# Kernel tuning notes

Hardware: AMD Instinct MI355X
Metric: run time of the kernel (lower is better)

## Reference

```python
import jax, jax.numpy as jnp
import numpy as np

N = 100000        # nodes
E = 1600000       # directed edges (before self loops)
F = 128           # input node features
H1, H2, H3 = 64, 32, 16
G = 64            # graphs in batch
EPS = 1e-5
NEG_SLOPE = 0.2


def setup_inputs():
    key = jax.random.key(0)
    ks = jax.random.split(key, 16)
    def rn(k, shape, scale=1.0):
        return jax.random.normal(k, shape, dtype=jnp.float32) * scale
    inp = {}
    inp['x'] = rn(ks[0], (N, F))
    inp['edge_index'] = jax.random.randint(ks[1], (2, E), 0, N)
    inp['batch'] = jnp.sort(jax.random.randint(ks[2], (N,), 0, G))
    dims = [(F, H1), (H1, H2), (H2, H3)]
    i = 3
    for li, (fi, fo) in enumerate(dims, start=1):
        s = 1.0 / np.sqrt(fi)
        kk = jax.random.split(ks[i], 3)
        inp[f'Wl{li}'] = rn(kk[0], (fi, fo), s)
        inp[f'bl{li}'] = jnp.zeros((fo,), jnp.float32)
        inp[f'Wr{li}'] = rn(kk[1], (fi, fo), s)
        inp[f'br{li}'] = jnp.zeros((fo,), jnp.float32)
        inp[f'att{li}'] = rn(kk[2], (fo,), 1.0 / np.sqrt(fo))
        inp[f'bias{li}'] = jnp.zeros((fo,), jnp.float32)
        inp[f'gamma{li}'] = jnp.ones((fo,), jnp.float32)
        inp[f'beta{li}'] = jnp.zeros((fo,), jnp.float32)
        i += 1
    inp['linW'] = rn(ks[i], (H3, 1), 0.25)
    inp['linb'] = jnp.zeros((1,), jnp.float32)
    return inp


def _gatv2(x, Wl, bl, Wr, br, att, bias, src, dst):
    # PyG GATv2Conv, heads=1: e_ij = a^T LeakyReLU(Wl x_j + Wr x_i)
    xl = x @ Wl + bl                         # [N, H] source transform
    xr = x @ Wr + br                         # [N, H] target transform
    e = jax.nn.leaky_relu(xl[src] + xr[dst], NEG_SLOPE) @ att   # [E']
    # numerically stable segment softmax over incoming edges of dst
    emax = jax.ops.segment_max(e, dst, num_segments=N)
    w = jnp.exp(e - emax[dst])
    denom = jax.ops.segment_sum(w, dst, num_segments=N)
    alpha = w / (denom[dst] + 1e-16)         # [E']
    out = jax.ops.segment_sum(alpha[:, None] * xl[src], dst, num_segments=N)
    return out + bias


def _batchnorm(x, gamma, beta):
    mu = jnp.mean(x, axis=0)
    var = jnp.var(x, axis=0)
    return (x - mu) * jax.lax.rsqrt(var + EPS) * gamma + beta


def reference(x, edge_index, batch,
              Wl1, bl1, Wr1, br1, att1, bias1, gamma1, beta1,
              Wl2, bl2, Wr2, br2, att2, bias2, gamma2, beta2,
              Wl3, bl3, Wr3, br3, att3, bias3, gamma3, beta3,
              linW, linb):
    # add self loops once (PyG GATv2Conv default add_self_loops=True)
    loops = jnp.arange(N, dtype=edge_index.dtype)
    src = jnp.concatenate([edge_index[0], loops])
    dst = jnp.concatenate([edge_index[1], loops])

    h = _gatv2(x, Wl1, bl1, Wr1, br1, att1, bias1, src, dst)
    h = jax.nn.relu(_batchnorm(h, gamma1, beta1))
    h = _gatv2(h, Wl2, bl2, Wr2, br2, att2, bias2, src, dst)
    h = jax.nn.relu(_batchnorm(h, gamma2, beta2))
    h = _gatv2(h, Wl3, bl3, Wr3, br3, att3, bias3, src, dst)
    h = jax.nn.relu(_batchnorm(h, gamma3, beta3))

    # global mean pool over graphs
    sums = jax.ops.segment_sum(h, batch, num_segments=G)          # [G, 16]
    cnts = jax.ops.segment_sum(jnp.ones((N,), h.dtype), batch, num_segments=G)
    pooled = sums / jnp.maximum(cnts, 1.0)[:, None]
    return pooled @ linW + linb                                   # [G, 1]
```

## Files before the change

kernel.cpp:

```cpp
#include <hip/hip_runtime.h>
#include <hip/hip_bf16.h>


static constexpr int G_ = 64;

typedef short bfrag __attribute__((ext_vector_type(8)));
typedef float facc  __attribute__((ext_vector_type(4)));

__device__ __forceinline__ float asfloat_(unsigned int u) {
  union { unsigned int i; float f; } c; c.i = u; return c.f;
}
__device__ __forceinline__ unsigned short f2bf(float f) {
  union { float f; unsigned int i; } c;
  c.f = f;
  unsigned int r = c.i + 0x7FFFu + ((c.i >> 16) & 1u);
  return (unsigned short)(r >> 16);
}

__device__ __forceinline__ void load_bf4(const unsigned short* p, float* f) {
  uint2 q = *reinterpret_cast<const uint2*>(p);
  f[0] = asfloat_(q.x << 16); f[1] = asfloat_(q.x & 0xFFFF0000u);
  f[2] = asfloat_(q.y << 16); f[3] = asfloat_(q.y & 0xFFFF0000u);
}

__global__ __launch_bounds__(256) void pack_all(
    const float* __restrict__ Wl1, const float* __restrict__ Wr1,
    const float* __restrict__ bl1, const float* __restrict__ br1,
    const float* __restrict__ Wl2, const float* __restrict__ Wr2,
    const float* __restrict__ bl2, const float* __restrict__ br2,
    const float* __restrict__ Wl3, const float* __restrict__ Wr3,
    const float* __restrict__ bl3, const float* __restrict__ br3,
    unsigned short* __restrict__ Wt1, float* __restrict__ bc1,
    unsigned short* __restrict__ Wt2, float* __restrict__ bc2,
    unsigned short* __restrict__ Wt3, float* __restrict__ bc3) {
  int i = blockIdx.x * 256 + threadIdx.x;
  if (i < 128 * 128) { int c = i >> 7, k = i & 127;
    Wt1[i] = f2bf((c < 64) ? Wl1[k * 64 + c] : Wr1[k * 64 + (c - 64)]); }
  if (i < 128) bc1[i] = (i < 64) ? bl1[i] : br1[i - 64];
  if (i < 64 * 64) { int c = i >> 6, k = i & 63;
    Wt2[i] = f2bf((c < 32) ? Wl2[k * 32 + c] : Wr2[k * 32 + (c - 32)]); }
  if (i < 64) bc2[i] = (i < 32) ? bl2[i] : br2[i - 32];
  if (i < 32 * 32) { int c = i >> 5, k = i & 31;
    Wt3[i] = f2bf((c < 16) ? Wl3[k * 16 + c] : Wr3[k * 16 + (c - 16)]); }
  if (i < 32) bc3[i] = (i < 16) ? bl3[i] : br3[i - 16];
}

__global__ __launch_bounds__(256) void edge_hist(
    const int* __restrict__ ei, int* __restrict__ deg, int E, int Etot, int N) {
  int p = blockIdx.x & 7;
  int q = blockIdx.x >> 3;
  int nbq = gridDim.x >> 3;
  float scale = 8.0f / (float)N;
  for (int i = q * 256 + threadIdx.x; i < Etot; i += nbq * 256) {
    int dst = (i < E) ? ei[E + i] : (i - E);
    int pp = min((int)((float)dst * scale), 7);
    if (pp == p) atomicAdd(&deg[dst], 1);
  }
}

__global__ __launch_bounds__(256) void scan1(
    const int* __restrict__ deg, int* __restrict__ part, int* __restrict__ bsums, int n) {
  __shared__ int ts[256];
  int t = threadIdx.x, b = blockIdx.x;
  int base = b * 1024 + t * 4;
  int d[4];
#pragma unroll
  for (int q = 0; q < 4; q++) d[q] = (base + q < n) ? deg[base + q] : 0;
  int s = d[0] + d[1] + d[2] + d[3];
  ts[t] = s;
  __syncthreads();
  for (int o = 1; o < 256; o <<= 1) {
    int v = (t >= o) ? ts[t - o] : 0;
    __syncthreads();
    ts[t] += v;
    __syncthreads();
  }
  int incl = ts[t];
  if (t == 255) bsums[b] = incl;
  int run = incl - s;
#pragma unroll
  for (int q = 0; q < 4; q++) {
    if (base + q < n) part[base + q] = run;
    run += d[q];
  }
}

__global__ void scan2(int* bsums, int nb) {
  __shared__ int s[256];
  int t = threadIdx.x;
  int v = (t < nb) ? bsums[t] : 0;
  s[t] = v;
  __syncthreads();
  for (int o = 1; o < 256; o <<= 1) {
    int u = (t >= o) ? s[t - o] : 0;
    __syncthreads();
    s[t] += u;
    __syncthreads();
  }
  if (t < nb) bsums[t] = s[t] - v;
}

__global__ __launch_bounds__(256) void scan3(
    int* __restrict__ rp, int* __restrict__ cur, const int* __restrict__ bsums,
    int n, int Etot) {
  int i = blockIdx.x * 256 + threadIdx.x;
  if (i < n) {
    int v = rp[i] + bsums[i >> 10];
    rp[i] = v; cur[i] = v;
  }
  if (i == 0) rp[n] = Etot;
}

__global__ __launch_bounds__(256) void scatter_edges(
    const int* __restrict__ ei, int* __restrict__ cur, int* __restrict__ ssrc,
    int E, int Etot, int N) {
  int p = blockIdx.x & 7;
  int q = blockIdx.x >> 3;
  int nbq = gridDim.x >> 3;
  float scale = 8.0f / (float)N;
  for (int i = q * 256 + threadIdx.x; i < Etot; i += nbq * 256) {
    int dst = (i < E) ? ei[E + i] : (i - E);
    int pp = min((int)((float)dst * scale), 7);
    if (pp != p) continue;
    int src = (i < E) ? ei[i] : (i - E);
    int pos = atomicAdd(&cur[dst], 1);
    ssrc[pos] = src;
  }
}

template <int FI, int FO, int AMODE>
__global__ __launch_bounds__(256) void gemm_mfma(
    const void* __restrict__ Ain, const float* __restrict__ ssb,
    const unsigned short* __restrict__ Wt, const float* __restrict__ bcat,
    unsigned short* __restrict__ XL, unsigned short* __restrict__ XR, int N) {
  constexpr int NT = FO / 16;
  constexpr int KS = FI / 32;
  constexpr int H = FO / 2;
  int tid = threadIdx.x;
  int w = tid >> 6;
  int lr = tid & 15;
  int lg = (tid & 63) >> 4;
  int n0 = blockIdx.x * 64;
  int arow = min(n0 + w * 16 + lr, N - 1);

  facc acc[NT];
#pragma unroll
  for (int t = 0; t < NT; t++)
#pragma unroll
    for (int e = 0; e < 4; e++) acc[t][e] = 0.f;

#pragma unroll
  for (int ks = 0; ks < KS; ks++) {
    int k0 = ks * 32 + lg * 8;
    bfrag a;
    if constexpr (AMODE == 0) {
      const unsigned short* Ab = (const unsigned short*)Ain;
      a = *reinterpret_cast<const bfrag*>(&Ab[(size_t)arow * FI + k0]);
    } else {
      const float* Af = (const float*)Ain;
      const float* p = &Af[(size_t)arow * FI + k0];
      float4 lo = *reinterpret_cast<const float4*>(p);
      float4 hi = *reinterpret_cast<const float4*>(p + 4);
      float f[8] = {lo.x, lo.y, lo.z, lo.w, hi.x, hi.y, hi.z, hi.w};
      if constexpr (AMODE == 2) {
        float4 sc0 = *reinterpret_cast<const float4*>(&ssb[k0]);
        float4 sc1 = *reinterpret_cast<const float4*>(&ssb[k0 + 4]);
        float4 sh0 = *reinterpret_cast<const float4*>(&ssb[FI + k0]);
        float4 sh1 = *reinterpret_cast<const float4*>(&ssb[FI + k0 + 4]);
        float sc[8] = {sc0.x, sc0.y, sc0.z, sc0.w, sc1.x, sc1.y, sc1.z, sc1.w};
        float sh[8] = {sh0.x, sh0.y, sh0.z, sh0.w, sh1.x, sh1.y, sh1.z, sh1.w};
#pragma unroll
        for (int e = 0; e < 8; e++) f[e] = fmaxf(fmaf(f[e], sc[e], sh[e]), 0.f);
      }
      union { bfrag v; unsigned short u[8]; } cv;
#pragma unroll
      for (int e = 0; e < 8; e++) cv.u[e] = f2bf(f[e]);
      a = cv.v;
    }
#pragma unroll
    for (int t = 0; t < NT; t++) {
      bfrag b = *reinterpret_cast<const bfrag*>(&Wt[(size_t)(t * 16 + lr) * FI + k0]);
      acc[t] = __builtin_amdgcn_mfma_f32_16x16x32_bf16(a, b, acc[t], 0, 0, 0);
    }
  }

#pragma unroll
  for (int t = 0; t < NT; t++) {
    int col = t * 16 + lr;
    float bias = bcat[col];
    unsigned short* dstbuf = (t < NT / 2) ? XL : XR;
    int cc = (t < NT / 2) ? col : (col - H);
#pragma unroll
    for (int r = 0; r < 4; r++) {
      int n = n0 + w * 16 + lg * 4 + r;
      if (n < N) dstbuf[(size_t)n * H + cc] = f2bf(acc[t][r] + bias);
    }
  }
}

__device__ __forceinline__ float lrelu02(float z) {
  return fmaxf(z, 0.2f * z);
}

template <int H, bool UN2>
__global__ __launch_bounds__(256) void gat_agg4(
    const unsigned short* __restrict__ XL, const unsigned short* __restrict__ XR,
    const float* __restrict__ att, const float* __restrict__ bias,
    const int* __restrict__ rp, const int* __restrict__ ssrc,
    float* __restrict__ out, int N) {
  constexpr int L = H / 4;
  constexpr int C = 64 / L;
  constexpr int STEP = UN2 ? 2 * C : C;
  int v = blockIdx.x * 4 + (threadIdx.x >> 6);
  if (v >= N) return;
  int lane = threadIdx.x & 63;
  int fl = lane % L;
  int sub = lane / L;

  float xr[4];
  load_bf4(&XR[(size_t)v * H + fl * 4], xr);
  const float4 a4 = *reinterpret_cast<const float4*>(&att[fl * 4]);
  int beg = rp[v], end = rp[v + 1];

  float mA = -3.0e38f, dA = 0.f, accA[4] = {0.f, 0.f, 0.f, 0.f};
  float mB = -3.0e38f, dB = 0.f, accB[4] = {0.f, 0.f, 0.f, 0.f};

  auto edge = [&](int j, float& m, float& d, float (&acc)[4]) {
    int u = ssrc[j];
    float xl[4];
    load_bf4(&XL[(size_t)u * H + fl * 4], xl);
    float t = a4.x * lrelu02(xl[0] + xr[0]);
    t = fmaf(a4.y, lrelu02(xl[1] + xr[1]), t);
    t = fmaf(a4.z, lrelu02(xl[2] + xr[2]), t);
    t = fmaf(a4.w, lrelu02(xl[3] + xr[3]), t);
#pragma unroll
    for (int o = L / 2; o >= 1; o >>= 1) t += __shfl_xor(t, o);
    float diff = t - m;
    if (diff > 8.f) {
      float sc = __expf(-diff);
      d *= sc;
#pragma unroll
      for (int e = 0; e < 4; e++) acc[e] *= sc;
      m = t; diff = 0.f;
    }
    float w = __expf(diff);
    d += w;
#pragma unroll
    for (int e = 0; e < 4; e++) acc[e] = fmaf(w, xl[e], acc[e]);
  };

  for (int j = beg + sub; j < end; j += STEP) {
    edge(j, mA, dA, accA);
    if (UN2) {
      int j2 = j + C;
      if (j2 < end) edge(j2, mB, dB, accB);
    }
  }

  if (UN2) {
    float mn = fmaxf(mA, mB);
    float s1 = __expf(mA - mn), s2 = __expf(mB - mn);
    dA = dA * s1 + dB * s2;
#pragma unroll
    for (int e = 0; e < 4; e++) accA[e] = accA[e] * s1 + accB[e] * s2;
    mA = mn;
  }

#pragma unroll
  for (int o = L; o < 64; o <<= 1) {
    float mo = __shfl_xor(mA, o);
    float d2 = __shfl_xor(dA, o);
    float a0 = __shfl_xor(accA[0], o);
    float a1 = __shfl_xor(accA[1], o);
    float a2 = __shfl_xor(accA[2], o);
    float a3 = __shfl_xor(accA[3], o);
    float mn = fmaxf(mA, mo);
    float s1 = __expf(mA - mn), s2 = __expf(mo - mn);
    dA = dA * s1 + d2 * s2;
    accA[0] = accA[0] * s1 + a0 * s2;
    accA[1] = accA[1] * s1 + a1 * s2;
    accA[2] = accA[2] * s1 + a2 * s2;
    accA[3] = accA[3] * s1 + a3 * s2;
    mA = mn;
  }

  if (lane < L) {
    float inv = 1.f / (dA + 1e-16f);
    const float4 b4 = *reinterpret_cast<const float4*>(&bias[fl * 4]);
    float4 o4 = make_float4(fmaf(accA[0], inv, b4.x), fmaf(accA[1], inv, b4.y),
                            fmaf(accA[2], inv, b4.z), fmaf(accA[3], inv, b4.w));
    *reinterpret_cast<float4*>(&out[(size_t)v * H + fl * 4]) = o4;
  }
}

template <int H>
__global__ __launch_bounds__(256) void bn_stats(
    const float* __restrict__ X, float* __restrict__ stats, int N) {
  __shared__ float ls[256], ls2[256];
  int tid = threadIdx.x;
  int h = tid % H;
  constexpr int RPB = 256 / H;
  int r0 = blockIdx.x * RPB + tid / H;
  float s = 0.f, s2 = 0.f;
  for (int n = r0; n < N; n += gridDim.x * RPB) {
    float val = X[(size_t)n * H + h];
    s += val; s2 += val * val;
  }
  ls[tid] = s; ls2[tid] = s2;
  __syncthreads();
  if (tid < H) {
    for (int g = 1; g < RPB; g++) { s += ls[tid + g * H]; s2 += ls2[tid + g * H]; }
    atomicAdd(&stats[h], s);
    atomicAdd(&stats[H + h], s2);
  }
}

__global__ void bn_finalize(
    const float* __restrict__ stats, const float* __restrict__ gamma,
    const float* __restrict__ beta, float* __restrict__ ss, int H, int N) {
  int h = threadIdx.x;
  if (h < H) {
    float mean = stats[h] / (float)N;
    float var = stats[H + h] / (float)N - mean * mean;
    float istd = rsqrtf(var + 1e-5f);
    float sc = gamma[h] * istd;
    ss[h] = sc;
    ss[H + h] = beta[h] - mean * sc;
  }
}

__global__ __launch_bounds__(256) void pool_kernel(
    const float* __restrict__ X, const float* __restrict__ ss,
    const int* __restrict__ batch, float* __restrict__ pool,
    float* __restrict__ cnt, int N) {
  __shared__ float lp[G_ * 16];
  __shared__ float lc[G_];
  int tid = threadIdx.x;
  for (int j = tid; j < G_ * 16; j += 256) lp[j] = 0.f;
  if (tid < G_) lc[tid] = 0.f;
  __syncthreads();
  int tot = N * 16;
  for (int i = blockIdx.x * 256 + tid; i < tot; i += gridDim.x * 256) {
    int n = i >> 4, h = i & 15;
    int g = batch[n];
    float t = X[i] * ss[h] + ss[16 + h];
    t = (t > 0.f) ? t : 0.f;
    atomicAdd(&lp[g * 16 + h], t);
    if (h == 0) atomicAdd(&lc[g], 1.0f);
  }
  __syncthreads();
  for (int j = tid; j < G_ * 16; j += 256) atomicAdd(&pool[j], lp[j]);
  if (tid < G_) atomicAdd(&cnt[tid], lc[tid]);
}

__global__ void final_linear(
    const float* __restrict__ pool, const float* __restrict__ cnt,
    const float* __restrict__ linW, const float* __restrict__ linb,
    float* __restrict__ out) {
  int g = threadIdx.x;
  if (g < G_) {
    float c = fmaxf(cnt[g], 1.0f);
    float acc = 0.f;
    for (int h = 0; h < 16; h++) acc += (pool[g * 16 + h] / c) * linW[h];
    out[g] = acc + linb[0];
  }
}

extern "C" void kernel_launch(void* const* d_in, const int* in_sizes, int n_in,
                              void* d_out, int out_size, void* d_ws, size_t ws_size,
                              hipStream_t stream) {
  const float* x = (const float*)d_in[0];
  const int* ei = (const int*)d_in[1];
  const int* batch = (const int*)d_in[2];
  const int N = in_sizes[0] / 128;
  const int E = in_sizes[1] / 2;
  const int Etot = E + N;

  char* wsb = (char*)d_ws;
  size_t off = 0;
  auto alloc = [&](size_t bytes) -> void* {
    void* p = wsb + off;
    off += (bytes + 255) & ~(size_t)255;
    return p;
  };
  unsigned short* XLb = (unsigned short*)alloc((size_t)64 * N * 2);
  unsigned short* XRb = (unsigned short*)alloc((size_t)64 * N * 2);
  float* R2 = (float*)alloc((size_t)64 * N * 4);
  int* row_ptr = (int*)alloc((size_t)(N + 1) * 4);
  int* cursor = (int*)alloc((size_t)N * 4);
  int* bsums = (int*)alloc(4096);
  int* ssrc = (int*)alloc((size_t)Etot * 4);
  unsigned short* Wt1 = (unsigned short*)alloc(16384 * 2);
  float* bc1 = (float*)alloc(128 * 4);
  unsigned short* Wt2 = (unsigned short*)alloc(4096 * 2);
  float* bc2 = (float*)alloc(64 * 4);
  unsigned short* Wt3 = (unsigned short*)alloc(1024 * 2);
  float* bc3 = (float*)alloc(32 * 4);
  float* ss = (float*)alloc(256 * 4);
  size_t zelems = (size_t)N + 3 * 128 + G_ * 16 + G_;
  char* zb = (char*)alloc(zelems * 4);
  int* deg = (int*)zb;
  float* stats1 = (float*)(zb + (size_t)N * 4);
  float* stats2 = stats1 + 128;
  float* stats3 = stats2 + 128;
  float* pool = stats3 + 128;
  float* cnt = pool + G_ * 16;

  const float* Wl1 = (const float*)d_in[3];  const float* bl1 = (const float*)d_in[4];
  const float* Wr1 = (const float*)d_in[5];  const float* br1 = (const float*)d_in[6];
  const float* att1 = (const float*)d_in[7]; const float* bias1 = (const float*)d_in[8];
  const float* g1 = (const float*)d_in[9];   const float* b1 = (const float*)d_in[10];
  const float* Wl2 = (const float*)d_in[11]; const float* bl2 = (const float*)d_in[12];
  const float* Wr2 = (const float*)d_in[13]; const float* br2 = (const float*)d_in[14];
  const float* att2 = (const float*)d_in[15]; const float* bias2 = (const float*)d_in[16];
  const float* g2 = (const float*)d_in[17];  const float* b2 = (const float*)d_in[18];
  const float* Wl3 = (const float*)d_in[19]; const float* bl3 = (const float*)d_in[20];
  const float* Wr3 = (const float*)d_in[21]; const float* br3 = (const float*)d_in[22];
  const float* att3 = (const float*)d_in[23]; const float* bias3 = (const float*)d_in[24];
  const float* g3 = (const float*)d_in[25];  const float* b3 = (const float*)d_in[26];
  const float* linW = (const float*)d_in[27]; const float* linb = (const float*)d_in[28];
  float* out = (float*)d_out;

  int nb = (N + 1023) / 1024;
  int nnodeblk = (N + 3) / 4;
  int ngemm = (N + 63) / 64;

  pack_all<<<64, 256, 0, stream>>>(Wl1, Wr1, bl1, br1, Wl2, Wr2, bl2, br2,
                                   Wl3, Wr3, bl3, br3, Wt1, bc1, Wt2, bc2, Wt3, bc3);
  hipMemsetAsync(zb, 0, zelems * 4, stream);

  edge_hist<<<4096, 256, 0, stream>>>(ei, deg, E, Etot, N);
  scan1<<<nb, 256, 0, stream>>>(deg, row_ptr, bsums, N);
  scan2<<<1, 256, 0, stream>>>(bsums, nb);
  scan3<<<(N + 255) / 256, 256, 0, stream>>>(row_ptr, cursor, bsums, N, Etot);
  scatter_edges<<<4096, 256, 0, stream>>>(ei, cursor, ssrc, E, Etot, N);

  gemm_mfma<128, 128, 1><<<ngemm, 256, 0, stream>>>(x, nullptr, Wt1, bc1, XLb, XRb, N);
  gat_agg4<64, true><<<nnodeblk, 256, 0, stream>>>(XLb, XRb, att1, bias1, row_ptr, ssrc, R2, N);
  bn_stats<64><<<512, 256, 0, stream>>>(R2, stats1, N);
  bn_finalize<<<1, 64, 0, stream>>>(stats1, g1, b1, ss, 64, N);

  gemm_mfma<64, 64, 2><<<ngemm, 256, 0, stream>>>(R2, ss, Wt2, bc2, XLb, XRb, N);
  gat_agg4<32, true><<<nnodeblk, 256, 0, stream>>>(XLb, XRb, att2, bias2, row_ptr, ssrc, R2, N);
  bn_stats<32><<<512, 256, 0, stream>>>(R2, stats2, N);
  bn_finalize<<<1, 64, 0, stream>>>(stats2, g2, b2, ss, 32, N);

  gemm_mfma<32, 32, 2><<<ngemm, 256, 0, stream>>>(R2, ss, Wt3, bc3, XLb, XRb, N);
  gat_agg4<16, false><<<nnodeblk, 256, 0, stream>>>(XLb, XRb, att3, bias3, row_ptr, ssrc, R2, N);
  bn_stats<16><<<512, 256, 0, stream>>>(R2, stats3, N);
  bn_finalize<<<1, 64, 0, stream>>>(stats3, g3, b3, ss, 16, N);

  pool_kernel<<<2048, 256, 0, stream>>>(R2, ss, batch, pool, cnt, N);
  final_linear<<<1, 64, 0, stream>>>(pool, cnt, linW, linb, out);
}
```

Measured before the change: 510.1 us.

## Replace online softmax in GAT aggregation with chunked two-pass LDS softmax

```diff
diff --git a/kernel.cpp b/kernel.cpp
--- a/kernel.cpp
+++ b/kernel.cpp
@@ -202,16 +202,18 @@
   return fmaxf(z, 0.2f * z);
 }
 
-template <int H, bool UN2>
-__global__ __launch_bounds__(256) void gat_agg4(
+template <int H>
+__global__ __launch_bounds__(256) void gat_agg5(
     const unsigned short* __restrict__ XL, const unsigned short* __restrict__ XR,
     const float* __restrict__ att, const float* __restrict__ bias,
     const int* __restrict__ rp, const int* __restrict__ ssrc,
     float* __restrict__ out, int N) {
   constexpr int L = H / 4;
   constexpr int C = 64 / L;
-  constexpr int STEP = UN2 ? 2 * C : C;
-  int v = blockIdx.x * 4 + (threadIdx.x >> 6);
+  constexpr int CHUNK = 128;
+  __shared__ float ts[4][CHUNK];
+  int wv = threadIdx.x >> 6;
+  int v = blockIdx.x * 4 + wv;
   if (v >= N) return;
   int lane = threadIdx.x & 63;
   int fl = lane % L;
@@ -222,73 +224,66 @@
   const float4 a4 = *reinterpret_cast<const float4*>(&att[fl * 4]);
   int beg = rp[v], end = rp[v + 1];
 
-  float mA = -3.0e38f, dA = 0.f, accA[4] = {0.f, 0.f, 0.f, 0.f};
-  float mB = -3.0e38f, dB = 0.f, accB[4] = {0.f, 0.f, 0.f, 0.f};
-
-  auto edge = [&](int j, float& m, float& d, float (&acc)[4]) {
-    int u = ssrc[j];
-    float xl[4];
-    load_bf4(&XL[(size_t)u * H + fl * 4], xl);
-    float t = a4.x * lrelu02(xl[0] + xr[0]);
-    t = fmaf(a4.y, lrelu02(xl[1] + xr[1]), t);
-    t = fmaf(a4.z, lrelu02(xl[2] + xr[2]), t);
-    t = fmaf(a4.w, lrelu02(xl[3] + xr[3]), t);
-#pragma unroll
-    for (int o = L / 2; o >= 1; o >>= 1) t += __shfl_xor(t, o);
-    float diff = t - m;
-    if (diff > 8.f) {
-      float sc = __expf(-diff);
-      d *= sc;
-#pragma unroll
-      for (int e = 0; e < 4; e++) acc[e] *= sc;
-      m = t; diff = 0.f;
-    }
-    float w = __expf(diff);
-    d += w;
-#pragma unroll
-    for (int e = 0; e < 4; e++) acc[e] = fmaf(w, xl[e], acc[e]);
-  };
-
-  for (int j = beg + sub; j < end; j += STEP) {
-    edge(j, mA, dA, accA);
-    if (UN2) {
-      int j2 = j + C;
-      if (j2 < end) edge(j2, mB, dB, accB);
-    }
-  }
-
-  if (UN2) {
-    float mn = fmaxf(mA, mB);
-    float s1 = __expf(mA - mn), s2 = __expf(mB - mn);
-    dA = dA * s1 + dB * s2;
-#pragma unroll
-    for (int e = 0; e < 4; e++) accA[e] = accA[e] * s1 + accB[e] * s2;
-    mA = mn;
+  float m = -3.0e38f, d = 0.f, acc[4] = {0.f, 0.f, 0.f, 0.f};
+
+  for (int c0 = beg; c0 < end; c0 += CHUNK) {
+    int n = min(CHUNK, end - c0);
+
+    float mc = -3.0e38f;
+    for (int k = sub; k < n; k += C) {
+      int u = ssrc[c0 + k];
+      float xl[4];
+      load_bf4(&XL[(size_t)u * H + fl * 4], xl);
+      float t = a4.x * lrelu02(xl[0] + xr[0]);
+      t = fmaf(a4.y, lrelu02(xl[1] + xr[1]), t);
+      t = fmaf(a4.z, lrelu02(xl[2] + xr[2]), t);
+      t = fmaf(a4.w, lrelu02(xl[3] + xr[3]), t);
+#pragma unroll
+      for (int o = L / 2; o >= 1; o >>= 1) t += __shfl_xor(t, o);
+      mc = fmaxf(mc, t);
+      if (fl == 0) ts[wv][k] = t;
+    }
+#pragma unroll
+    for (int o = L; o < 64; o <<= 1) mc = fmaxf(mc, __shfl_xor(mc, o));
+
+    float mn = fmaxf(m, mc);
+    float sc = __expf(m - mn);
+    d *= sc;
+#pragma unroll
+    for (int e = 0; e < 4; e++) acc[e] *= sc;
+    m = mn;
+
+    float dl = 0.f;
+    for (int k = lane; k < n; k += 64) {
+      float w = __expf(ts[wv][k] - m);
+      ts[wv][k] = w;
+      dl += w;
+    }
+#pragma unroll
+    for (int o = 1; o < 64; o <<= 1) dl += __shfl_xor(dl, o);
+    d += dl;
+
+    for (int k = sub; k < n; k += C) {
+      float wgt = ts[wv][k];
+      int u = ssrc[c0 + k];
+      float xl[4];
+      load_bf4(&XL[(size_t)u * H + fl * 4], xl);
+#pragma unroll
+      for (int e = 0; e < 4; e++) acc[e] = fmaf(wgt, xl[e], acc[e]);
+    }
   }
 
 #pragma unroll
   for (int o = L; o < 64; o <<= 1) {
-    float mo = __shfl_xor(mA, o);
-    float d2 = __shfl_xor(dA, o);
-    float a0 = __shfl_xor(accA[0], o);
-    float a1 = __shfl_xor(accA[1], o);
-    float a2 = __shfl_xor(accA[2], o);
-    float a3 = __shfl_xor(accA[3], o);
-    float mn = fmaxf(mA, mo);
-    float s1 = __expf(mA - mn), s2 = __expf(mo - mn);
-    dA = dA * s1 + d2 * s2;
-    accA[0] = accA[0] * s1 + a0 * s2;
-    accA[1] = accA[1] * s1 + a1 * s2;
-    accA[2] = accA[2] * s1 + a2 * s2;
-    accA[3] = accA[3] * s1 + a3 * s2;
-    mA = mn;
+#pragma unroll
+    for (int e = 0; e < 4; e++) acc[e] += __shfl_xor(acc[e], o);
   }
 
   if (lane < L) {
-    float inv = 1.f / (dA + 1e-16f);
+    float inv = 1.f / (d + 1e-16f);
     const float4 b4 = *reinterpret_cast<const float4*>(&bias[fl * 4]);
-    float4 o4 = make_float4(fmaf(accA[0], inv, b4.x), fmaf(accA[1], inv, b4.y),
-                            fmaf(accA[2], inv, b4.z), fmaf(accA[3], inv, b4.w));
+    float4 o4 = make_float4(fmaf(acc[0], inv, b4.x), fmaf(acc[1], inv, b4.y),
+                            fmaf(acc[2], inv, b4.z), fmaf(acc[3], inv, b4.w));
     *reinterpret_cast<float4*>(&out[(size_t)v * H + fl * 4]) = o4;
   }
 }
@@ -436,17 +431,17 @@
   scatter_edges<<<4096, 256, 0, stream>>>(ei, cursor, ssrc, E, Etot, N);
 
   gemm_mfma<128, 128, 1><<<ngemm, 256, 0, stream>>>(x, nullptr, Wt1, bc1, XLb, XRb, N);
-  gat_agg4<64, true><<<nnodeblk, 256, 0, stream>>>(XLb, XRb, att1, bias1, row_ptr, ssrc, R2, N);
+  gat_agg5<64><<<nnodeblk, 256, 0, stream>>>(XLb, XRb, att1, bias1, row_ptr, ssrc, R2, N);
   bn_stats<64><<<512, 256, 0, stream>>>(R2, stats1, N);
   bn_finalize<<<1, 64, 0, stream>>>(stats1, g1, b1, ss, 64, N);
 
   gemm_mfma<64, 64, 2><<<ngemm, 256, 0, stream>>>(R2, ss, Wt2, bc2, XLb, XRb, N);
-  gat_agg4<32, true><<<nnodeblk, 256, 0, stream>>>(XLb, XRb, att2, bias2, row_ptr, ssrc, R2, N);
+  gat_agg5<32><<<nnodeblk, 256, 0, stream>>>(XLb, XRb, att2, bias2, row_ptr, ssrc, R2, N);
   bn_stats<32><<<512, 256, 0, stream>>>(R2, stats2, N);
   bn_finalize<<<1, 64, 0, stream>>>(stats2, g2, b2, ss, 32, N);
 
   gemm_mfma<32, 32, 2><<<ngemm, 256, 0, stream>>>(R2, ss, Wt3, bc3, XLb, XRb, N);
-  gat_agg4<16, false><<<nnodeblk, 256, 0, stream>>>(XLb, XRb, att3, bias3, row_ptr, ssrc, R2, N);
+  gat_agg5<16><<<nnodeblk, 256, 0, stream>>>(XLb, XRb, att3, bias3, row_ptr, ssrc, R2, N);
   bn_stats<16><<<512, 256, 0, stream>>>(R2, stats3, N);
   bn_finalize<<<1, 64, 0, stream>>>(stats3, g3, b3, ss, 16, N);
 
```

After: 578.3 us. +13.4%, slower.

## Add chunked batch-load GAT aggregation kernel for layers two and three

Applied to the files above, without the earlier changes.

```diff
diff --git a/kernel.cpp b/kernel.cpp
--- a/kernel.cpp
+++ b/kernel.cpp
@@ -152,31 +152,26 @@
 #pragma unroll
   for (int ks = 0; ks < KS; ks++) {
     int k0 = ks * 32 + lg * 8;
+    const float* Af = (const float*)Ain;
+    const float* p = &Af[(size_t)arow * FI + k0];
+    float4 lo = *reinterpret_cast<const float4*>(p);
+    float4 hi = *reinterpret_cast<const float4*>(p + 4);
+    float f[8] = {lo.x, lo.y, lo.z, lo.w, hi.x, hi.y, hi.z, hi.w};
+    if constexpr (AMODE == 2) {
+      float4 sc0 = *reinterpret_cast<const float4*>(&ssb[k0]);
+      float4 sc1 = *reinterpret_cast<const float4*>(&ssb[k0 + 4]);
+      float4 sh0 = *reinterpret_cast<const float4*>(&ssb[FI + k0]);
+      float4 sh1 = *reinterpret_cast<const float4*>(&ssb[FI + k0 + 4]);
+      float sc[8] = {sc0.x, sc0.y, sc0.z, sc0.w, sc1.x, sc1.y, sc1.z, sc1.w};
+      float sh[8] = {sh0.x, sh0.y, sh0.z, sh0.w, sh1.x, sh1.y, sh1.z, sh1.w};
+#pragma unroll
+      for (int e = 0; e < 8; e++) f[e] = fmaxf(fmaf(f[e], sc[e], sh[e]), 0.f);
+    }
     bfrag a;
-    if constexpr (AMODE == 0) {
-      const unsigned short* Ab = (const unsigned short*)Ain;
-      a = *reinterpret_cast<const bfrag*>(&Ab[(size_t)arow * FI + k0]);
-    } else {
-      const float* Af = (const float*)Ain;
-      const float* p = &Af[(size_t)arow * FI + k0];
-      float4 lo = *reinterpret_cast<const float4*>(p);
-      float4 hi = *reinterpret_cast<const float4*>(p + 4);
-      float f[8] = {lo.x, lo.y, lo.z, lo.w, hi.x, hi.y, hi.z, hi.w};
-      if constexpr (AMODE == 2) {
-        float4 sc0 = *reinterpret_cast<const float4*>(&ssb[k0]);
-        float4 sc1 = *reinterpret_cast<const float4*>(&ssb[k0 + 4]);
-        float4 sh0 = *reinterpret_cast<const float4*>(&ssb[FI + k0]);
-        float4 sh1 = *reinterpret_cast<const float4*>(&ssb[FI + k0 + 4]);
-        float sc[8] = {sc0.x, sc0.y, sc0.z, sc0.w, sc1.x, sc1.y, sc1.z, sc1.w};
-        float sh[8] = {sh0.x, sh0.y, sh0.z, sh0.w, sh1.x, sh1.y, sh1.z, sh1.w};
-#pragma unroll
-        for (int e = 0; e < 8; e++) f[e] = fmaxf(fmaf(f[e], sc[e], sh[e]), 0.f);
-      }
-      union { bfrag v; unsigned short u[8]; } cv;
-#pragma unroll
-      for (int e = 0; e < 8; e++) cv.u[e] = f2bf(f[e]);
-      a = cv.v;
-    }
+    union { bfrag v; unsigned short u[8]; } cv;
+#pragma unroll
+    for (int e = 0; e < 8; e++) cv.u[e] = f2bf(f[e]);
+    a = cv.v;
 #pragma unroll
     for (int t = 0; t < NT; t++) {
       bfrag b = *reinterpret_cast<const bfrag*>(&Wt[(size_t)(t * 16 + lr) * FI + k0]);
@@ -202,7 +197,7 @@
   return fmaxf(z, 0.2f * z);
 }
 
-template <int H, bool UN2>
+template <int H>
 __global__ __launch_bounds__(256) void gat_agg4(
     const unsigned short* __restrict__ XL, const unsigned short* __restrict__ XR,
     const float* __restrict__ att, const float* __restrict__ bias,
@@ -210,7 +205,7 @@
     float* __restrict__ out, int N) {
   constexpr int L = H / 4;
   constexpr int C = 64 / L;
-  constexpr int STEP = UN2 ? 2 * C : C;
+  constexpr int STEP = 2 * C;
   int v = blockIdx.x * 4 + (threadIdx.x >> 6);
   if (v >= N) return;
   int lane = threadIdx.x & 63;
@@ -251,13 +246,11 @@
 
   for (int j = beg + sub; j < end; j += STEP) {
     edge(j, mA, dA, accA);
-    if (UN2) {
-      int j2 = j + C;
-      if (j2 < end) edge(j2, mB, dB, accB);
-    }
-  }
-
-  if (UN2) {
+    int j2 = j + C;
+    if (j2 < end) edge(j2, mB, dB, accB);
+  }
+
+  {
     float mn = fmaxf(mA, mB);
     float s1 = __expf(mA - mn), s2 = __expf(mB - mn);
     dA = dA * s1 + dB * s2;
@@ -289,6 +282,83 @@
     const float4 b4 = *reinterpret_cast<const float4*>(&bias[fl * 4]);
     float4 o4 = make_float4(fmaf(accA[0], inv, b4.x), fmaf(accA[1], inv, b4.y),
                             fmaf(accA[2], inv, b4.z), fmaf(accA[3], inv, b4.w));
+    *reinterpret_cast<float4*>(&out[(size_t)v * H + fl * 4]) = o4;
+  }
+}
+
+template <int H, int ITER>
+__global__ __launch_bounds__(256) void gat_agg6(
+    const unsigned short* __restrict__ XL, const unsigned short* __restrict__ XR,
+    const float* __restrict__ att, const float* __restrict__ bias,
+    const int* __restrict__ rp, const int* __restrict__ ssrc,
+    float* __restrict__ out, int N) {
+  constexpr int L = H / 4;
+  constexpr int C = 64 / L;
+  constexpr int CHUNK = C * ITER;
+  int v = blockIdx.x * 4 + (threadIdx.x >> 6);
+  if (v >= N) return;
+  int lane = threadIdx.x & 63;
+  int fl = lane % L;
+  int sub = lane / L;
+
+  float xr[4];
+  load_bf4(&XR[(size_t)v * H + fl * 4], xr);
+  const float4 a4 = *reinterpret_cast<const float4*>(&att[fl * 4]);
+  int beg = rp[v], end = rp[v + 1];
+
+  float m = -3.0e38f, d = 0.f, acc[4] = {0.f, 0.f, 0.f, 0.f};
+
+  for (int cb = beg; cb < end; cb += CHUNK) {
+    float xb[ITER][4];
+    float tl[ITER];
+    float mc = -3.0e38f;
+#pragma unroll
+    for (int it = 0; it < ITER; it++) {
+      int j = cb + it * C + sub;
+      bool valid = (j < end);
+      int jj = valid ? j : (end - 1);
+      int u = ssrc[jj];
+      load_bf4(&XL[(size_t)u * H + fl * 4], xb[it]);
+      float t = a4.x * lrelu02(xb[it][0] + xr[0]);
+      t = fmaf(a4.y, lrelu02(xb[it][1] + xr[1]), t);
+      t = fmaf(a4.z, lrelu02(xb[it][2] + xr[2]), t);
+      t = fmaf(a4.w, lrelu02(xb[it][3] + xr[3]), t);
+#pragma unroll
+      for (int o = L / 2; o >= 1; o >>= 1) t += __shfl_xor(t, o);
+      tl[it] = valid ? t : -3.0e38f;
+      mc = fmaxf(mc, tl[it]);
+    }
+#pragma unroll
+    for (int o = L; o < 64; o <<= 1) mc = fmaxf(mc, __shfl_xor(mc, o));
+
+    float mn = fmaxf(m, mc);
+    float sc = __expf(m - mn);
+    d *= sc;
+#pragma unroll
+    for (int e = 0; e < 4; e++) acc[e] *= sc;
+    m = mn;
+
+#pragma unroll
+    for (int it = 0; it < ITER; it++) {
+      float w = __expf(tl[it] - m);
+      d += w;
+#pragma unroll
+      for (int e = 0; e < 4; e++) acc[e] = fmaf(w, xb[it][e], acc[e]);
+    }
+  }
+
+#pragma unroll
+  for (int o = L; o < 64; o <<= 1) {
+    d += __shfl_xor(d, o);
+#pragma unroll
+    for (int e = 0; e < 4; e++) acc[e] += __shfl_xor(acc[e], o);
+  }
+
+  if (lane < L) {
+    float inv = 1.f / (d + 1e-16f);
+    const float4 b4 = *reinterpret_cast<const float4*>(&bias[fl * 4]);
+    float4 o4 = make_float4(fmaf(acc[0], inv, b4.x), fmaf(acc[1], inv, b4.y),
+                            fmaf(acc[2], inv, b4.z), fmaf(acc[3], inv, b4.w));
     *reinterpret_cast<float4*>(&out[(size_t)v * H + fl * 4]) = o4;
   }
 }
@@ -436,17 +506,17 @@
   scatter_edges<<<4096, 256, 0, stream>>>(ei, cursor, ssrc, E, Etot, N);
 
   gemm_mfma<128, 128, 1><<<ngemm, 256, 0, stream>>>(x, nullptr, Wt1, bc1, XLb, XRb, N);
-  gat_agg4<64, true><<<nnodeblk, 256, 0, stream>>>(XLb, XRb, att1, bias1, row_ptr, ssrc, R2, N);
+  gat_agg4<64><<<nnodeblk, 256, 0, stream>>>(XLb, XRb, att1, bias1, row_ptr, ssrc, R2, N);
   bn_stats<64><<<512, 256, 0, stream>>>(R2, stats1, N);
   bn_finalize<<<1, 64, 0, stream>>>(stats1, g1, b1, ss, 64, N);
 
   gemm_mfma<64, 64, 2><<<ngemm, 256, 0, stream>>>(R2, ss, Wt2, bc2, XLb, XRb, N);
-  gat_agg4<32, true><<<nnodeblk, 256, 0, stream>>>(XLb, XRb, att2, bias2, row_ptr, ssrc, R2, N);
+  gat_agg6<32, 4><<<nnodeblk, 256, 0, stream>>>(XLb, XRb, att2, bias2, row_ptr, ssrc, R2, N);
   bn_stats<32><<<512, 256, 0, stream>>>(R2, stats2, N);
   bn_finalize<<<1, 64, 0, stream>>>(stats2, g2, b2, ss, 32, N);
 
   gemm_mfma<32, 32, 2><<<ngemm, 256, 0, stream>>>(R2, ss, Wt3, bc3, XLb, XRb, N);
-  gat_agg4<16, false><<<nnodeblk, 256, 0, stream>>>(XLb, XRb, att3, bias3, row_ptr, ssrc, R2, N);
+  gat_agg6<16, 2><<<nnodeblk, 256, 0, stream>>>(XLb, XRb, att3, bias3, row_ptr, ssrc, R2, N);
   bn_stats<16><<<512, 256, 0, stream>>>(R2, stats3, N);
   bn_finalize<<<1, 64, 0, stream>>>(stats3, g3, b3, ss, 16, N);
 
```

Measured after the change: 500.6 us. About the same (-1.9%).
